# Optimization experiments

Measured on AMD Instinct MI355X. Metric: run time of the kernel, lower is better.

Reference implementation:

```python
import jax, jax.numpy as jnp
import numpy as np

B, L, D = 2, 2048, 2048
H, KV, HD = 16, 8, 128
EPS = 1e-5
ROPE_BASE = 10000.0
SCALING_ALPHA = 1.0
SCALE = HD ** -0.5


def setup_inputs() -> dict:
    key = jax.random.key(0)
    ks = jax.random.split(key, 5)
    s = 0.02  # weight init scale
    return {
        "x": jax.random.normal(ks[0], (B, L, D), jnp.float32),
        "wq": jax.random.normal(ks[1], (D, H * HD), jnp.float32) * s,
        "wk": jax.random.normal(ks[2], (D, KV * HD), jnp.float32) * s,
        "wv": jax.random.normal(ks[3], (D, KV * HD), jnp.float32) * s,
        "wo": jax.random.normal(ks[4], (H * HD, D), jnp.float32) * s,
        "qn_w": jnp.ones((HD,), jnp.float32),
        "kn_w": jnp.ones((HD,), jnp.float32),
    }


def _rope(t):
    # t: [B, h, L, HD]. DynamicNTKAlpha base scaling (alpha=1 -> no-op).
    base = ROPE_BASE * SCALING_ALPHA ** (HD / (HD - 2))
    # NOTE: source uses base**(+i/d) (no negative exponent) -- kept faithful.
    freqs = base ** (jnp.arange(0, HD, 2, dtype=jnp.float32) / HD)  # [HD/2]
    pos = jnp.arange(t.shape[-2], dtype=jnp.float32)                # [L]
    angles = pos[:, None] * freqs[None, :]                          # [L, HD/2]
    cos, sin = jnp.cos(angles), jnp.sin(angles)
    x1, x2 = t[..., : HD // 2], t[..., HD // 2 :]
    return jnp.concatenate([x1 * cos - x2 * sin, x2 * cos + x1 * sin], axis=-1)


def _rmsnorm(t, w):
    return t * jax.lax.rsqrt(jnp.mean(t * t, axis=-1, keepdims=True) + EPS) * w


def reference(x, wq, wk, wv, wo, qn_w, kn_w):
    b, l, _ = x.shape
    q = (x @ wq).reshape(b, l, H, HD).transpose(0, 2, 1, 3)   # [B,H,L,HD]
    k = (x @ wk).reshape(b, l, KV, HD).transpose(0, 2, 1, 3)  # [B,KV,L,HD]
    v = (x @ wv).reshape(b, l, KV, HD).transpose(0, 2, 1, 3)
    q = _rmsnorm(_rope(q), qn_w)
    k = _rmsnorm(_rope(k), kn_w)
    # GQA: expand KV heads to match query heads
    rep = H // KV
    k = jnp.repeat(k, rep, axis=1)  # [B,H,L,HD]
    v = jnp.repeat(v, rep, axis=1)
    scores = jnp.einsum("bhqd,bhkd->bhqk", q, k) * SCALE
    probs = jax.nn.softmax(scores, axis=-1)
    out = jnp.einsum("bhqk,bhkd->bhqd", probs, v)             # [B,H,L,HD]
    out = out.transpose(0, 2, 1, 3).reshape(b, l, H * HD)
    return out @ wo
```

## Files before the change

kernel.cpp:

```cpp
#include <hip/hip_runtime.h>
#include <math.h>

#define BB 2
#define LL 2048
#define DD 2048
#define HH 16
#define KVH 8
#define HDIM 128
#define SCALE_F 0.08838834764831845f
#define EPS_F 1e-5f
#define LOG2E 1.4426950408889634f
#define SMAX_F 17.0f
#define QKVW 4096

typedef unsigned short u16;
typedef __attribute__((ext_vector_type(8))) short short8;
typedef __attribute__((ext_vector_type(4))) float f32x4;
typedef __attribute__((ext_vector_type(16))) float f32x16;

#define MFMA16(a, b, c) __builtin_amdgcn_mfma_f32_16x16x32_bf16((a), (b), (c), 0, 0, 0)
#define MFMA32(a, b, c) __builtin_amdgcn_mfma_f32_32x32x16_bf16((a), (b), (c), 0, 0, 0)

__device__ __forceinline__ float b2f(u16 u) {
    union { unsigned int i; float f; } x;
    x.i = ((unsigned int)u) << 16;
    return x.f;
}
__device__ __forceinline__ u16 f2b(float f) {
    unsigned int x = __float_as_uint(f);
    unsigned int r = x + 0x7FFFu + ((x >> 16) & 1u);
    return (u16)(r >> 16);
}
__device__ __forceinline__ unsigned cvtpk(float lo, float hi) {
    unsigned r;
    asm("v_cvt_pk_bf16_f32 %0, %1, %2" : "=v"(r) : "v"(lo), "v"(hi));
    return r;
}
__device__ __forceinline__ void pl32swap(unsigned &a, unsigned &b) {
    asm("v_permlane32_swap_b32 %0, %1" : "+v"(a), "+v"(b));
}
__device__ __forceinline__ void g2l(const u16* g, u16* l) {
    __builtin_amdgcn_global_load_lds(
        (const __attribute__((address_space(1))) unsigned int*)g,
        (__attribute__((address_space(3))) unsigned int*)l, 16, 0, 0);
}

__global__ __launch_bounds__(256) void prep_kernel(const float* __restrict__ x,
                                                   u16* __restrict__ xb,
                                                   const float* __restrict__ wq,
                                                   const float* __restrict__ wk,
                                                   const float* __restrict__ wv,
                                                   const float* __restrict__ wo,
                                                   u16* __restrict__ wqkvT,
                                                   u16* __restrict__ woT,
                                                   float* __restrict__ ct,
                                                   float* __restrict__ st) {
    __shared__ u16 t[64 * 65];
    const int blk = blockIdx.x, tid = threadIdx.x;
    if (blk < 8192) {
        int i = (blk * 256 + tid) * 4;
        float4 v = *(const float4*)(x + i);
        unsigned int p0 = (unsigned int)f2b(v.x) | ((unsigned int)f2b(v.y) << 16);
        unsigned int p1 = (unsigned int)f2b(v.z) | ((unsigned int)f2b(v.w) << 16);
        uint2 pk; pk.x = p0; pk.y = p1;
        *(uint2*)(xb + i) = pk;
    } else if (blk < 11264) {
        int j = blk - 8192;
        const float* in; u16* out; int C, bx, by;
        if (j < 1024)      { in = wq; out = wqkvT;                      C = 2048; bx = j & 31; by = j >> 5; }
        else if (j < 1536) { j -= 1024; in = wk; out = wqkvT + (size_t)2048 * DD; C = 1024; bx = j & 15; by = j >> 4; }
        else if (j < 2048) { j -= 1536; in = wv; out = wqkvT + (size_t)3072 * DD; C = 1024; bx = j & 15; by = j >> 4; }
        else               { j -= 2048; in = wo; out = woT;                      C = 2048; bx = j & 31; by = j >> 5; }
        int c0 = bx * 64, r0 = by * 64;
#pragma unroll
        for (int i = 0; i < 16; i++) {
            int idx = tid + i * 256;
            int r = idx >> 6, c = idx & 63;
            t[r * 65 + c] = f2b(in[(size_t)(r0 + r) * C + c0 + c]);
        }
        __syncthreads();
#pragma unroll
        for (int i = 0; i < 16; i++) {
            int idx = tid + i * 256;
            int r = idx >> 6, c = idx & 63;
            out[(size_t)(c0 + r) * DD + r0 + c] = t[c * 65 + r];
        }
    } else {
        int i = (blk - 11264) * 256 + tid;
        int pos = i >> 6, d = i & 63;
        float freq = (float)pow(10000.0, (double)d * (1.0 / 64.0));
        float ang = (float)pos * freq;
        double a = (double)ang;
        ct[i] = (float)cos(a);
        st[i] = (float)sin(a);
    }
}

__global__ __launch_bounds__(256) void gemm_bt(const u16* __restrict__ A,
                                               const u16* __restrict__ Bt,
                                               u16* __restrict__ C, int M, int N, int K) {
    __shared__ __align__(16) u16 As[128 * 64];
    __shared__ __align__(16) u16 Bs[128 * 64];
    const int tid = threadIdx.x;
    const int w = tid >> 6, lane = tid & 63;
    const int lm = lane & 15, lq = lane >> 4;
    const int bn0 = blockIdx.x * 128, bm0 = blockIdx.y * 128;
    const int wm = (w >> 1) * 64, wn = (w & 1) * 64;

    f32x4 acc[4][4];
#pragma unroll
    for (int i = 0; i < 4; i++)
#pragma unroll
        for (int j = 0; j < 4; j++) acc[i][j] = (f32x4){0.f, 0.f, 0.f, 0.f};

    const int srow = lane >> 3;
    const int sgr = (lane & 7) ^ (srow & 7);
    const u16* ga = A + (size_t)(bm0 + w * 32 + srow) * K + sgr * 8;
    const u16* gb = Bt + (size_t)(bn0 + w * 32 + srow) * K + sgr * 8;
    u16* lA = &As[(w * 32) * 64];
    u16* lB = &Bs[(w * 32) * 64];

    for (int k0 = 0; k0 < K; k0 += 64) {
        __syncthreads();
#pragma unroll
        for (int ch = 0; ch < 4; ch++)
            g2l(ga + (size_t)(ch * 8) * K + k0, lA + ch * 8 * 64);
#pragma unroll
        for (int ch = 0; ch < 4; ch++)
            g2l(gb + (size_t)(ch * 8) * K + k0, lB + ch * 8 * 64);
        __syncthreads();

#pragma unroll
        for (int sub = 0; sub < 2; sub++) {
            short8 af[4], bf[4];
#pragma unroll
            for (int mt = 0; mt < 4; mt++) {
                int row = wm + mt * 16 + lm;
                af[mt] = *(const short8*)(&As[row * 64 + ((sub * 4 + lq) ^ (lm & 7)) * 8]);
            }
#pragma unroll
            for (int nt = 0; nt < 4; nt++) {
                int row = wn + nt * 16 + lm;
                bf[nt] = *(const short8*)(&Bs[row * 64 + ((sub * 4 + lq) ^ (lm & 7)) * 8]);
            }
#pragma unroll
            for (int mt = 0; mt < 4; mt++)
#pragma unroll
                for (int nt = 0; nt < 4; nt++) acc[mt][nt] = MFMA16(af[mt], bf[nt], acc[mt][nt]);
        }
    }

#pragma unroll
    for (int mt = 0; mt < 4; mt++)
#pragma unroll
        for (int nt = 0; nt < 4; nt++)
#pragma unroll
            for (int r = 0; r < 4; r++) {
                int row = bm0 + wm + mt * 16 + lq * 4 + r;
                int col = bn0 + wn + nt * 16 + lm;
                C[(size_t)row * N + col] = f2b(acc[mt][nt][r]);
            }
}

__global__ __launch_bounds__(256) void gemm_bt_o(const u16* __restrict__ A,
                                                 const u16* __restrict__ Bt,
                                                 float* __restrict__ C, int M, int N, int K) {
    __shared__ __align__(16) u16 As[64 * 64];
    __shared__ __align__(16) u16 Bs[128 * 64];
    const int tid = threadIdx.x;
    const int w = tid >> 6, lane = tid & 63;
    const int lm = lane & 15, lq = lane >> 4;
    const int bn0 = blockIdx.x * 128, bm0 = blockIdx.y * 64;
    const int wm = (w >> 1) * 32, wn = (w & 1) * 64;

    f32x4 acc[2][4];
#pragma unroll
    for (int i = 0; i < 2; i++)
#pragma unroll
        for (int j = 0; j < 4; j++) acc[i][j] = (f32x4){0.f, 0.f, 0.f, 0.f};

    const int srow = lane >> 3;
    const int sgr = (lane & 7) ^ (srow & 7);
    const u16* ga = A + (size_t)(bm0 + w * 16 + srow) * K + sgr * 8;
    const u16* gb = Bt + (size_t)(bn0 + w * 32 + srow) * K + sgr * 8;
    u16* lA = &As[(w * 16) * 64];
    u16* lB = &Bs[(w * 32) * 64];

    for (int k0 = 0; k0 < K; k0 += 64) {
        __syncthreads();
#pragma unroll
        for (int ch = 0; ch < 2; ch++)
            g2l(ga + (size_t)(ch * 8) * K + k0, lA + ch * 8 * 64);
#pragma unroll
        for (int ch = 0; ch < 4; ch++)
            g2l(gb + (size_t)(ch * 8) * K + k0, lB + ch * 8 * 64);
        __syncthreads();

#pragma unroll
        for (int sub = 0; sub < 2; sub++) {
            short8 af[2], bf[4];
#pragma unroll
            for (int mt = 0; mt < 2; mt++) {
                int row = wm + mt * 16 + lm;
                af[mt] = *(const short8*)(&As[row * 64 + ((sub * 4 + lq) ^ (lm & 7)) * 8]);
            }
#pragma unroll
            for (int nt = 0; nt < 4; nt++) {
                int row = wn + nt * 16 + lm;
                bf[nt] = *(const short8*)(&Bs[row * 64 + ((sub * 4 + lq) ^ (lm & 7)) * 8]);
            }
#pragma unroll
            for (int mt = 0; mt < 2; mt++)
#pragma unroll
                for (int nt = 0; nt < 4; nt++) acc[mt][nt] = MFMA16(af[mt], bf[nt], acc[mt][nt]);
        }
    }

#pragma unroll
    for (int mt = 0; mt < 2; mt++)
#pragma unroll
        for (int nt = 0; nt < 4; nt++)
#pragma unroll
            for (int r = 0; r < 4; r++) {
                int row = bm0 + wm + mt * 16 + lq * 4 + r;
                int col = bn0 + wn + nt * 16 + lm;
                C[(size_t)row * N + col] = acc[mt][nt][r];
            }
}

__global__ __launch_bounds__(256) void ropetv_kernel(u16* __restrict__ qkv,
                                                     u16* __restrict__ vt,
                                                     const float* __restrict__ qw,
                                                     const float* __restrict__ kw,
                                                     const float* __restrict__ ct,
                                                     const float* __restrict__ st) {
    __shared__ u16 t[64 * 65];
    const int blk = blockIdx.x, tid = threadIdx.x;
    if (blk < 24576) {
        int slot = blk * 4 + (tid >> 6);
        int lane = tid & 63;
        int hh = slot % (HH + KVH);
        int row = slot / (HH + KVH);
        int pos = row & (LL - 1);

        u16* base = qkv + (size_t)row * QKVW + hh * HDIM;
        const float* w = (hh < HH) ? qw : kw;

        float x1 = b2f(base[lane]), x2 = b2f(base[lane + 64]);
        float c = ct[pos * 64 + lane], s = st[pos * 64 + lane];
        float r1 = x1 * c - x2 * s;
        float r2 = x2 * c + x1 * s;
        float ss = r1 * r1 + r2 * r2;
#pragma unroll
        for (int m = 1; m < 64; m <<= 1) ss += __shfl_xor(ss, m, 64);
        float sc = 1.0f / sqrtf(ss * (1.0f / 128.0f) + EPS_F);
        base[lane] = f2b(r1 * sc * w[lane]);
        base[lane + 64] = f2b(r2 * sc * w[lane + 64]);
    } else {
        int j = blk - 24576;
        int bx = j & 31, by = (j >> 5) & 1, bg = j >> 6;
        int l0 = bx * 64, d0 = by * 64;
        int b = bg >> 3, g = bg & 7;
        const u16* src = qkv + (size_t)b * LL * QKVW + 3072 + g * HDIM;
        u16* dst = vt + (size_t)bg * HDIM * LL;
#pragma unroll
        for (int i = 0; i < 16; i++) {
            int idx = tid + i * 256;
            int r = idx >> 6, c = idx & 63;
            t[r * 65 + c] = src[(size_t)(l0 + r) * QKVW + d0 + c];
        }
        __syncthreads();
#pragma unroll
        for (int i = 0; i < 16; i++) {
            int idx = tid + i * 256;
            int r = idx >> 6, c = idx & 63;
            dst[(size_t)(d0 + r) * LL + l0 + c] = t[c * 65 + r];
        }
    }
}

__global__ __launch_bounds__(256, 3) void attn_kernel(const u16* __restrict__ qkv,
                                                      const u16* __restrict__ vt,
                                                      u16* __restrict__ ob) {
    __shared__ __align__(16) u16 SM[2 * 64 * 128 + 128 * 64];
    u16* Vt = SM + 2 * 64 * 128;

    const int tid = threadIdx.x, w = tid >> 6, lane = tid & 63;
    const int l31 = lane & 31, lh = lane >> 5;
    const int qh = w & 1, kh = w >> 1;

    const int bid = blockIdx.y * 32 + blockIdx.x;
    const int xcd = bid & 7, idx = bid >> 3;
    const int bh = xcd * 4 + (idx >> 5);
    const int q0 = (idx & 31) * 64;
    const int b = bh >> 4, hd = bh & 15, g = hd >> 1;

    const u16* kbase = qkv + (size_t)b * LL * QKVW + 2048 + g * HDIM;
    const u16* vtbase = vt + (size_t)(b * KVH + g) * HDIM * LL;

    const int krl = lane >> 4, kgl = lane & 15;
    const int vrl = lane >> 3, vgl = lane & 7;

#define STAGEK(tt, bi) do {                                                  \
        _Pragma("unroll")                                                    \
        for (int ch = 0; ch < 4; ch++) {                                     \
            int r_ = w * 16 + ch * 4 + krl;                                  \
            int gc_ = kgl ^ (r_ & 15);                                       \
            g2l(kbase + (size_t)((tt) * 64 + r_) * QKVW + gc_ * 8,           \
                SM + (bi) * 8192 + (w * 16 + ch * 4) * 128);                 \
        }                                                                    \
    } while (0)
#define STAGEV(tt) do {                                                      \
        _Pragma("unroll")                                                    \
        for (int ch = 0; ch < 4; ch++) {                                     \
            int r_ = w * 32 + ch * 8 + vrl;                                  \
            int gc_ = vgl ^ (r_ & 7);                                        \
            g2l(vtbase + (size_t)r_ * LL + (tt) * 64 + gc_ * 8,              \
                Vt + (w * 32 + ch * 8) * 64);                                \
        }                                                                    \
    } while (0)

    const int qrow = q0 + qh * 32 + l31;
    short8 aq[8];
    {
        const u16* qp = qkv + (size_t)(b * LL + qrow) * QKVW + hd * HDIM + lh * 8;
#pragma unroll
        for (int kk = 0; kk < 8; kk++) aq[kk] = *(const short8*)(qp + kk * 16);
    }

    f32x16 o[4];
#pragma unroll
    for (int i = 0; i < 4; i++)
#pragma unroll
        for (int r = 0; r < 16; r++) o[i][r] = 0.f;
    float psum = 0.f;
    const float SC2 = SCALE_F * LOG2E;
    const f32x16 fz = {};

    STAGEK(0, 0);
    asm volatile("s_waitcnt vmcnt(0)" ::: "memory");
    __builtin_amdgcn_s_barrier();

    for (int t = 0; t < LL / 64; t++) {
        const int cur = t & 1;
        const u16* Kc = SM + cur * 8192;
        STAGEV(t);
        STAGEK((t + 1) & (LL / 64 - 1), cur ^ 1);

        const int key = kh * 32 + l31;
        f32x16 s;
        __builtin_amdgcn_s_setprio(1);
        {
            int gg = lh ^ (key & 15);
            short8 kf = *(const short8*)(&Kc[key * 128 + gg * 8]);
            s = MFMA32(kf, aq[0], fz);
        }
#pragma unroll
        for (int kk = 1; kk < 8; kk++) {
            int gg = (kk * 2 + lh) ^ (key & 15);
            short8 kf = *(const short8*)(&Kc[key * 128 + gg * 8]);
            s = MFMA32(kf, aq[kk], s);
        }
        __builtin_amdgcn_s_setprio(0);

        float p[16];
#pragma unroll
        for (int r = 0; r < 16; r++) {
            p[r] = __builtin_amdgcn_exp2f(fmaf(s[r], SC2, -SMAX_F));
            psum += p[r];
        }
        unsigned pw[2][4];
#pragma unroll
        for (int half = 0; half < 2; half++) {
            int qb = half * 8;
            unsigned c0 = cvtpk(p[qb + 0], p[qb + 1]);
            unsigned c1 = cvtpk(p[qb + 2], p[qb + 3]);
            unsigned c2 = cvtpk(p[qb + 4], p[qb + 5]);
            unsigned c3 = cvtpk(p[qb + 6], p[qb + 7]);
            pl32swap(c0, c2);
            pl32swap(c1, c3);
            pw[half][0] = c0; pw[half][1] = c1; pw[half][2] = c2; pw[half][3] = c3;
        }

        asm volatile("s_waitcnt vmcnt(4)" ::: "memory");
        __builtin_amdgcn_s_barrier();

        __builtin_amdgcn_s_setprio(1);
#pragma unroll
        for (int kcl = 0; kcl < 2; kcl++) {
            int kc = kh * 2 + kcl;
            union { unsigned u[4]; short8 s8; } pu;
#pragma unroll
            for (int i = 0; i < 4; i++) pu.u[i] = pw[kcl][i];
#pragma unroll
            for (int dn = 0; dn < 4; dn++) {
                int d = dn * 32 + l31;
                int gv = ((kc * 2 + lh) ^ (d & 7)) * 8;
                short8 bv = *(const short8*)(&Vt[d * 64 + gv]);
                o[dn] = MFMA32(pu.s8, bv, o[dn]);
            }
        }
        __builtin_amdgcn_s_setprio(0);

        asm volatile("s_waitcnt vmcnt(0)" ::: "memory");
        __builtin_amdgcn_s_barrier();
    }
#undef STAGEK
#undef STAGEV

    psum += __shfl_xor(psum, 32, 64);

    __syncthreads();
    float* xo = (float*)SM;
    float* xp = xo + 2 * 64 * 68;
    if (kh == 1) {
        float* dst = xo + (qh * 64 + lane) * 68;
#pragma unroll
        for (int dn = 0; dn < 4; dn++)
#pragma unroll
            for (int r = 0; r < 16; r += 4)
                *(f32x4*)(dst + dn * 16 + r) =
                    (f32x4){o[dn][r], o[dn][r + 1], o[dn][r + 2], o[dn][r + 3]};
        xp[qh * 64 + lane] = psum;
    }
    __syncthreads();
    if (kh == 0) {
        const float* src = xo + (qh * 64 + lane) * 68;
        float inv = 1.0f / (psum + xp[qh * 64 + lane]);
        float invr[16];
#pragma unroll
        for (int r = 0; r < 16; r++) {
            int row = (r & 3) + 8 * (r >> 2) + 4 * lh;
            invr[r] = __shfl(inv, row, 32);
        }
        u16* obase = ob + (size_t)(b * LL + q0 + qh * 32) * (HH * HDIM) + hd * HDIM;
#pragma unroll
        for (int dn = 0; dn < 4; dn++)
#pragma unroll
            for (int r = 0; r < 16; r++) {
                int row = (r & 3) + 8 * (r >> 2) + 4 * lh;
                float v = o[dn][r] + src[dn * 16 + r];
                obase[(size_t)row * (HH * HDIM) + dn * 32 + l31] = f2b(v * invr[r]);
            }
    }
}

extern "C" void kernel_launch(void* const* d_in, const int* in_sizes, int n_in,
                              void* d_out, int out_size, void* d_ws, size_t ws_size,
                              hipStream_t stream) {
    const float* x  = (const float*)d_in[0];
    const float* wq = (const float*)d_in[1];
    const float* wk = (const float*)d_in[2];
    const float* wv = (const float*)d_in[3];
    const float* wo = (const float*)d_in[4];
    const float* qn = (const float*)d_in[5];
    const float* kn = (const float*)d_in[6];

    u16* ws = (u16*)d_ws;
    const size_t SZ_X = (size_t)BB * LL * DD;
    u16* xb    = ws;
    u16* qkv   = xb + SZ_X;
    u16* wqkvT = qkv + (size_t)BB * LL * QKVW;
    u16* woT   = wqkvT + (size_t)QKVW * DD;
    float* ct  = (float*)(woT + (size_t)DD * DD);
    float* st  = ct + (size_t)LL * 64;
    u16* att = xb;
    u16* vt  = wqkvT;

    prep_kernel<<<dim3(11776), dim3(256), 0, stream>>>(x, xb, wq, wk, wv, wo,
                                                       wqkvT, woT, ct, st);
    gemm_bt<<<dim3(QKVW / 128, BB * LL / 128), dim3(256), 0, stream>>>(xb, wqkvT, qkv, BB * LL, QKVW, DD);
    ropetv_kernel<<<dim3(25600), dim3(256), 0, stream>>>(qkv, vt, qn, kn, ct, st);
    attn_kernel<<<dim3(LL / 64, BB * HH), dim3(256), 0, stream>>>(qkv, vt, att);
    gemm_bt_o<<<dim3(DD / 128, BB * LL / 64), dim3(256), 0, stream>>>(att, woT, (float*)d_out, BB * LL, DD, DD);
}
```

Measured before the change: 358.5 us.

## Swizzle GEMM block order per XCD and split QK MFMA chain into two accumulators

Both projection GEMMs now remap the linear block id so that each XCD works on a contiguous 2D patch of output tiles, aiming for better L2 reuse of A and B tiles within an XCD. In the attention kernel, the serial chain of 8 dependent 32x32 MFMAs for QK^T is split into two independent accumulators that are summed before the exp, which should hide MFMA dependency latency. The P-fragment packing also goes through a union so the extra register copy disappears. The costs are a few extra VALU adds per tile and a remap that assumes a fixed grid shape.

Result: slower. 399.0 us (+11.3%).

```diff
diff --git a/kernel.cpp b/kernel.cpp
--- a/kernel.cpp
+++ b/kernel.cpp
@@ -104,7 +104,11 @@
     const int tid = threadIdx.x;
     const int w = tid >> 6, lane = tid & 63;
     const int lm = lane & 15, lq = lane >> 4;
-    const int bn0 = blockIdx.x * 128, bm0 = blockIdx.y * 128;
+    const int bid = blockIdx.y * 32 + blockIdx.x;
+    const int xcd = bid & 7, idx = bid >> 3;
+    const int bx = (xcd & 3) * 8 + (idx & 7);
+    const int by = (xcd >> 2) * 16 + (idx >> 3);
+    const int bn0 = bx * 128, bm0 = by * 128;
     const int wm = (w >> 1) * 64, wn = (w & 1) * 64;
 
     f32x4 acc[4][4];
@@ -170,7 +174,11 @@
     const int tid = threadIdx.x;
     const int w = tid >> 6, lane = tid & 63;
     const int lm = lane & 15, lq = lane >> 4;
-    const int bn0 = blockIdx.x * 128, bm0 = blockIdx.y * 64;
+    const int bid = blockIdx.y * 16 + blockIdx.x;
+    const int xcd = bid & 7, idx = bid >> 3;
+    const int bx = (xcd & 1) * 8 + (idx & 7);
+    const int by = (xcd >> 1) * 16 + (idx >> 3);
+    const int bn0 = bx * 128, bm0 = by * 64;
     const int wm = (w >> 1) * 32, wn = (w & 1) * 64;
 
     f32x4 acc[2][4];
@@ -348,28 +356,35 @@
         STAGEK((t + 1) & (LL / 64 - 1), cur ^ 1);
 
         const int key = kh * 32 + l31;
-        f32x16 s;
+        f32x16 sa, sb;
         __builtin_amdgcn_s_setprio(1);
         {
-            int gg = lh ^ (key & 15);
-            short8 kf = *(const short8*)(&Kc[key * 128 + gg * 8]);
-            s = MFMA32(kf, aq[0], fz);
-        }
-#pragma unroll
-        for (int kk = 1; kk < 8; kk++) {
-            int gg = (kk * 2 + lh) ^ (key & 15);
-            short8 kf = *(const short8*)(&Kc[key * 128 + gg * 8]);
-            s = MFMA32(kf, aq[kk], s);
+            int gg0 = lh ^ (key & 15);
+            short8 kf0 = *(const short8*)(&Kc[key * 128 + gg0 * 8]);
+            sa = MFMA32(kf0, aq[0], fz);
+            int gg1 = (2 + lh) ^ (key & 15);
+            short8 kf1 = *(const short8*)(&Kc[key * 128 + gg1 * 8]);
+            sb = MFMA32(kf1, aq[1], fz);
+        }
+#pragma unroll
+        for (int kk = 2; kk < 8; kk += 2) {
+            int gga = (kk * 2 + lh) ^ (key & 15);
+            short8 kfa = *(const short8*)(&Kc[key * 128 + gga * 8]);
+            sa = MFMA32(kfa, aq[kk], sa);
+            int ggb = ((kk + 1) * 2 + lh) ^ (key & 15);
+            short8 kfb = *(const short8*)(&Kc[key * 128 + ggb * 8]);
+            sb = MFMA32(kfb, aq[kk + 1], sb);
         }
         __builtin_amdgcn_s_setprio(0);
 
         float p[16];
 #pragma unroll
         for (int r = 0; r < 16; r++) {
-            p[r] = __builtin_amdgcn_exp2f(fmaf(s[r], SC2, -SMAX_F));
+            p[r] = __builtin_amdgcn_exp2f(fmaf(sa[r] + sb[r], SC2, -SMAX_F));
             psum += p[r];
         }
-        unsigned pw[2][4];
+        union PW { unsigned u[4]; short8 s8; };
+        PW pw[2];
 #pragma unroll
         for (int half = 0; half < 2; half++) {
             int qb = half * 8;
@@ -379,7 +394,8 @@
             unsigned c3 = cvtpk(p[qb + 6], p[qb + 7]);
             pl32swap(c0, c2);
             pl32swap(c1, c3);
-            pw[half][0] = c0; pw[half][1] = c1; pw[half][2] = c2; pw[half][3] = c3;
+            pw[half].u[0] = c0; pw[half].u[1] = c1;
+            pw[half].u[2] = c2; pw[half].u[3] = c3;
         }
 
         asm volatile("s_waitcnt vmcnt(4)" ::: "memory");
@@ -389,15 +405,12 @@
 #pragma unroll
         for (int kcl = 0; kcl < 2; kcl++) {
             int kc = kh * 2 + kcl;
-            union { unsigned u[4]; short8 s8; } pu;
-#pragma unroll
-            for (int i = 0; i < 4; i++) pu.u[i] = pw[kcl][i];
 #pragma unroll
             for (int dn = 0; dn < 4; dn++) {
                 int d = dn * 32 + l31;
                 int gv = ((kc * 2 + lh) ^ (d & 7)) * 8;
                 short8 bv = *(const short8*)(&Vt[d * 64 + gv]);
-                o[dn] = MFMA32(pu.s8, bv, o[dn]);
+                o[dn] = MFMA32(pw[kcl].s8, bv, o[dn]);
             }
         }
         __builtin_amdgcn_s_setprio(0);
```

## Fuse RoPE, RMSNorm and V transpose into QKV GEMM epilogue

Applied to the files above, without the earlier changes.

The QKV projection GEMM now stages its output tile in shared memory and applies RoPE plus RMSNorm to the Q and K head tiles before writing them out. For V tiles it writes the transposed layout directly. This removes the separate ropetv kernel launch and its extra global read and write pass over the QKV buffer. In exchange the GEMM gains a larger LDS footprint, extra syncs and a serial per-thread epilogue, and the V-transpose buffer moves to a separate workspace region.

Measured after the change: 353.9 us. No clear change (-1.3%).

```diff
diff --git a/kernel.cpp b/kernel.cpp
--- a/kernel.cpp
+++ b/kernel.cpp
@@ -96,11 +96,18 @@
     }
 }
 
-__global__ __launch_bounds__(256) void gemm_bt(const u16* __restrict__ A,
-                                               const u16* __restrict__ Bt,
-                                               u16* __restrict__ C, int M, int N, int K) {
-    __shared__ __align__(16) u16 As[128 * 64];
-    __shared__ __align__(16) u16 Bs[128 * 64];
+__global__ __launch_bounds__(256) void gemm_qkv(const u16* __restrict__ A,
+                                                const u16* __restrict__ Bt,
+                                                u16* __restrict__ qkv,
+                                                u16* __restrict__ vt,
+                                                const float* __restrict__ qw,
+                                                const float* __restrict__ kw,
+                                                const float* __restrict__ ct,
+                                                const float* __restrict__ st) {
+    __shared__ __align__(16) u16 SM[17408];
+    u16* As = SM;
+    u16* Bs = SM + 8192;
+    const int K = DD, N = QKVW;
     const int tid = threadIdx.x;
     const int w = tid >> 6, lane = tid & 63;
     const int lm = lane & 15, lq = lane >> 4;
@@ -150,16 +157,72 @@
         }
     }
 
+    __syncthreads();
+    u16* T = SM;
 #pragma unroll
     for (int mt = 0; mt < 4; mt++)
 #pragma unroll
         for (int nt = 0; nt < 4; nt++)
 #pragma unroll
             for (int r = 0; r < 4; r++) {
-                int row = bm0 + wm + mt * 16 + lq * 4 + r;
-                int col = bn0 + wn + nt * 16 + lm;
-                C[(size_t)row * N + col] = f2b(acc[mt][nt][r]);
-            }
+                int row = wm + mt * 16 + lq * 4 + r;
+                int col = wn + nt * 16 + lm;
+                T[row * 136 + col] = f2b(acc[mt][nt][r]);
+            }
+    __syncthreads();
+
+    const int bx = blockIdx.x;
+    const int row = tid >> 1, h = tid & 1;
+    if (bx < 24) {
+        const float* wgt = (bx < 16) ? qw : kw;
+        const int grow = bm0 + row;
+        const int pos = grow & (LL - 1);
+        const float* crow = ct + pos * 64 + h * 32;
+        const float* srw  = st + pos * 64 + h * 32;
+        const u16* t1 = &T[row * 136 + h * 32];
+        const u16* t2 = t1 + 64;
+        float ss = 0.f;
+#pragma unroll
+        for (int dd = 0; dd < 32; dd++) {
+            float x1 = b2f(t1[dd]), x2 = b2f(t2[dd]);
+            float c = crow[dd], s = srw[dd];
+            float r1 = x1 * c - x2 * s;
+            float r2 = x2 * c + x1 * s;
+            ss += r1 * r1 + r2 * r2;
+        }
+        ss += __shfl_xor(ss, 1, 64);
+        float sc = 1.0f / sqrtf(ss * (1.0f / 128.0f) + EPS_F);
+        u16* out = qkv + (size_t)grow * QKVW + bx * 128 + h * 32;
+#pragma unroll
+        for (int dd = 0; dd < 32; dd += 2) {
+            float x1a = b2f(t1[dd]),     x2a = b2f(t2[dd]);
+            float x1b = b2f(t1[dd + 1]), x2b = b2f(t2[dd + 1]);
+            float ca = crow[dd],     sa = srw[dd];
+            float cb = crow[dd + 1], sb = srw[dd + 1];
+            float r1a = x1a * ca - x2a * sa, r2a = x2a * ca + x1a * sa;
+            float r1b = x1b * cb - x2b * sb, r2b = x2b * cb + x1b * sb;
+            int d = h * 32 + dd;
+            unsigned p1 = (unsigned)f2b(r1a * sc * wgt[d]) |
+                          ((unsigned)f2b(r1b * sc * wgt[d + 1]) << 16);
+            unsigned p2 = (unsigned)f2b(r2a * sc * wgt[d + 64]) |
+                          ((unsigned)f2b(r2b * sc * wgt[d + 65]) << 16);
+            *(unsigned*)(out + dd) = p1;
+            *(unsigned*)(out + 64 + dd) = p2;
+        }
+    } else {
+        const int g = bx - 24;
+        const int b = bm0 >> 11;
+        const int d = row;
+        u16* dst = vt + ((size_t)(b * KVH + g) * HDIM + d) * LL +
+                   (bm0 & (LL - 1)) + h * 64;
+        const u16* src = &T[(h * 64) * 136 + d];
+#pragma unroll
+        for (int j = 0; j < 64; j += 2) {
+            unsigned pk = (unsigned)src[j * 136] |
+                          ((unsigned)src[(j + 1) * 136] << 16);
+            *(unsigned*)(dst + j) = pk;
+        }
+    }
 }
 
 __global__ __launch_bounds__(256) void gemm_bt_o(const u16* __restrict__ A,
@@ -226,57 +289,6 @@
                 int col = bn0 + wn + nt * 16 + lm;
                 C[(size_t)row * N + col] = acc[mt][nt][r];
             }
-}
-
-__global__ __launch_bounds__(256) void ropetv_kernel(u16* __restrict__ qkv,
-                                                     u16* __restrict__ vt,
-                                                     const float* __restrict__ qw,
-                                                     const float* __restrict__ kw,
-                                                     const float* __restrict__ ct,
-                                                     const float* __restrict__ st) {
-    __shared__ u16 t[64 * 65];
-    const int blk = blockIdx.x, tid = threadIdx.x;
-    if (blk < 24576) {
-        int slot = blk * 4 + (tid >> 6);
-        int lane = tid & 63;
-        int hh = slot % (HH + KVH);
-        int row = slot / (HH + KVH);
-        int pos = row & (LL - 1);
-
-        u16* base = qkv + (size_t)row * QKVW + hh * HDIM;
-        const float* w = (hh < HH) ? qw : kw;
-
-        float x1 = b2f(base[lane]), x2 = b2f(base[lane + 64]);
-        float c = ct[pos * 64 + lane], s = st[pos * 64 + lane];
-        float r1 = x1 * c - x2 * s;
-        float r2 = x2 * c + x1 * s;
-        float ss = r1 * r1 + r2 * r2;
-#pragma unroll
-        for (int m = 1; m < 64; m <<= 1) ss += __shfl_xor(ss, m, 64);
-        float sc = 1.0f / sqrtf(ss * (1.0f / 128.0f) + EPS_F);
-        base[lane] = f2b(r1 * sc * w[lane]);
-        base[lane + 64] = f2b(r2 * sc * w[lane + 64]);
-    } else {
-        int j = blk - 24576;
-        int bx = j & 31, by = (j >> 5) & 1, bg = j >> 6;
-        int l0 = bx * 64, d0 = by * 64;
-        int b = bg >> 3, g = bg & 7;
-        const u16* src = qkv + (size_t)b * LL * QKVW + 3072 + g * HDIM;
-        u16* dst = vt + (size_t)bg * HDIM * LL;
-#pragma unroll
-        for (int i = 0; i < 16; i++) {
-            int idx = tid + i * 256;
-            int r = idx >> 6, c = idx & 63;
-            t[r * 65 + c] = src[(size_t)(l0 + r) * QKVW + d0 + c];
-        }
-        __syncthreads();
-#pragma unroll
-        for (int i = 0; i < 16; i++) {
-            int idx = tid + i * 256;
-            int r = idx >> 6, c = idx & 63;
-            dst[(size_t)(d0 + r) * LL + l0 + c] = t[c * 65 + r];
-        }
-    }
 }
 
 __global__ __launch_bounds__(256, 3) void attn_kernel(const u16* __restrict__ qkv,
@@ -464,13 +476,13 @@
     u16* woT   = wqkvT + (size_t)QKVW * DD;
     float* ct  = (float*)(woT + (size_t)DD * DD);
     float* st  = ct + (size_t)LL * 64;
+    u16* vt    = (u16*)(st + (size_t)LL * 64);
     u16* att = xb;
-    u16* vt  = wqkvT;
 
     prep_kernel<<<dim3(11776), dim3(256), 0, stream>>>(x, xb, wq, wk, wv, wo,
                                                        wqkvT, woT, ct, st);
-    gemm_bt<<<dim3(QKVW / 128, BB * LL / 128), dim3(256), 0, stream>>>(xb, wqkvT, qkv, BB * LL, QKVW, DD);
-    ropetv_kernel<<<dim3(25600), dim3(256), 0, stream>>>(qkv, vt, qn, kn, ct, st);
+    gemm_qkv<<<dim3(QKVW / 128, BB * LL / 128), dim3(256), 0, stream>>>(
+        xb, wqkvT, qkv, vt, qn, kn, ct, st);
     attn_kernel<<<dim3(LL / 64, BB * HH), dim3(256), 0, stream>>>(qkv, vt, att);
     gemm_bt_o<<<dim3(DD / 128, BB * LL / 64), dim3(256), 0, stream>>>(att, woT, (float*)d_out, BB * LL, DD, DD);
 }
```
